# Kernel tuning notes

Measured on AMD Instinct MI355X. Metric: run time of the kernel, lower is better.

The kernel has to match this reference:

```python
import jax, jax.numpy as jnp
import numpy as np
from jax import lax

N = 4096        # num graph nodes
T = 8           # timesteps (LSTM batch dim in original, batch_first=False)
IN_DIM = 64
H = 128         # hidden_dim
OUT_DIM = 1
E_RAND = 65536  # random edges; self-loops appended -> E = 69632


def setup_inputs() -> dict:
    key = jax.random.key(0)
    ks = jax.random.split(key, 18)
    s = 0.05
    f = lambda k, shp: (jax.random.normal(k, shp, jnp.float32) * s)
    src = jnp.concatenate([jax.random.randint(ks[15], (E_RAND,), 0, N), jnp.arange(N)]).astype(jnp.int32)
    dst = jnp.concatenate([jax.random.randint(ks[16], (E_RAND,), 0, N), jnp.arange(N)]).astype(jnp.int32)
    return {
        "input": jax.random.normal(ks[0], (N, T, IN_DIM), jnp.float32),
        "hidden": f(ks[1], (1, T, H)),
        "cell": f(ks[2], (1, T, H)),
        "pre_w": f(ks[3], (IN_DIM, H)),
        "pre_b": f(ks[4], (H,)),
        "w_ih": f(ks[5], (4 * H, H)),
        "w_hh": f(ks[6], (4 * H, H)),
        "b_ih": f(ks[7], (4 * H,)),
        "b_hh": f(ks[8], (4 * H,)),
        "gat_wsrc": f(ks[9], (H, H)),
        "gat_wdst": f(ks[10], (H, H)),
        "gat_attn": f(ks[11], (H,)),
        "gat_b": f(ks[12], (H,)),
        "out_w": f(ks[13], (H, OUT_DIM)),
        "out_b": f(ks[14], (OUT_DIM,)),
        "edge_src": src,
        "edge_dst": dst,
    }


def reference(input, hidden, cell, pre_w, pre_b, w_ih, w_hh, b_ih, b_hh,
              gat_wsrc, gat_wdst, gat_attn, gat_b, out_w, out_b,
              edge_src, edge_dst):
    n_nodes = input.shape[0]
    x = input @ pre_w + pre_b                         # (N, T, H)
    b = b_ih + b_hh

    # LSTM over node dimension (seq = nodes); the T per-timestep runs of the
    # original Python loop are independent (init states come from the given
    # hidden/cell), so we batch them along T.
    def step(carry, x_n):                             # x_n: (T, H)
        h, c = carry
        g = x_n @ w_ih.T + h @ w_hh.T + b             # (T, 4H), torch gate order i,f,g,o
        i_g, f_g, g_g, o_g = jnp.split(g, 4, axis=-1)
        c = jax.nn.sigmoid(f_g) * c + jax.nn.sigmoid(i_g) * jnp.tanh(g_g)
        h = jax.nn.sigmoid(o_g) * jnp.tanh(c)
        return (h, c), h

    (hT, cT), outs = lax.scan(step, (hidden[0], cell[0]), x)   # outs: (N, T, H)

    # GATv2Conv (DGL semantics, num_heads=1, share_weights=False)
    fs = outs @ gat_wsrc                              # (N, T, H)
    fd = outs @ gat_wdst
    e = jax.nn.leaky_relu(fs[edge_src] + fd[edge_dst], 0.2)    # (E, T, H)
    logits = e @ gat_attn                             # (E, T)
    # edge softmax per destination node (numerically stable)
    m = lax.stop_gradient(jax.ops.segment_max(logits, edge_dst, num_segments=n_nodes))
    a = jnp.exp(logits - m[edge_dst])
    denom = jax.ops.segment_sum(a, edge_dst, num_segments=n_nodes)
    alpha = a / denom[edge_dst]                       # (E, T)
    agg = jax.ops.segment_sum(alpha[..., None] * fs[edge_src], edge_dst, num_segments=n_nodes)
    rst = agg + gat_b                                 # (N, T, H)

    # dropout is identity in eval mode
    y = rst @ out_w + out_b                           # (N, T, OUT_DIM)
    return (y, hT[None], cT[None])
```

## Files before the change

### kernel.cpp

```cpp
#include <hip/hip_runtime.h>
#include <hip/hip_bf16.h>

#define N_NODES 4096
#define T_STEPS 8
#define INDIM   64
#define HDIM    128
#define G4      512
#define NROWS   (N_NODES * T_STEPS)
#define LOG2E   1.4426950408889634f

typedef __hip_bfloat16 bf16;
typedef __attribute__((ext_vector_type(8))) short bf16x8;
typedef __attribute__((ext_vector_type(4))) float f32x4;
typedef __attribute__((ext_vector_type(8))) int   i32x8;

__device__ __forceinline__ float asfloat_u(unsigned int u) {
    union { unsigned int i; float f; } v; v.i = u; return v.f;
}
__device__ __forceinline__ float fexp2(float x) {
    float r; asm("v_exp_f32 %0, %1" : "=v"(r) : "v"(x)); return r;
}

#define P_O0 32768
#define P_O1 (P_O0 + 512)
#define P_O2 (P_O1 + 16384)
#define P_O3 (P_O2 + 16384)
#define P_O4 (P_O3 + 128)
#define P_O5 (P_O4 + 1)
#define P_O6 (P_O5 + 65536)
#define P_O7 (P_O6 + 128)
__global__ void prep_kernel(const float* __restrict__ pre_w, const float* __restrict__ pre_b,
                            const float* __restrict__ w_ih, const float* __restrict__ b_ih,
                            const float* __restrict__ b_hh, const float* __restrict__ w_hh,
                            const float* __restrict__ wsrc, const float* __restrict__ wdst,
                            const float* __restrict__ out_w, const float* __restrict__ out_b,
                            const float* __restrict__ gat_b, const float* __restrict__ attn,
                            float* __restrict__ Wc, float* __restrict__ bc,
                            float* __restrict__ wsT, float* __restrict__ wdT,
                            float* __restrict__ wso, float* __restrict__ cy,
                            unsigned char* __restrict__ whh8, float* __restrict__ attn2) {
    int id = blockIdx.x * 256 + threadIdx.x;
    if (id < P_O0) {
        int g = id >> 6, i = id & 63;
        float s = 0.f;
        for (int k = 0; k < HDIM; k++) s += pre_w[i * HDIM + k] * w_ih[g * HDIM + k];
        int gate = g >> 7;
        Wc[id] = s * ((gate == 2) ? -2.f * LOG2E : -LOG2E);
    } else if (id < P_O1) {
        int g = id - P_O0;
        float s = b_ih[g] + b_hh[g];
        for (int k = 0; k < HDIM; k++) s += pre_b[k] * w_ih[g * HDIM + k];
        int gate = g >> 7;
        bc[g] = s * ((gate == 2) ? -2.f * LOG2E : -LOG2E);
    } else if (id < P_O2) {
        int c = id - P_O1;
        int co = c >> 7, k = c & 127;
        wsT[c] = wsrc[k * HDIM + co];
    } else if (id < P_O3) {
        int c = id - P_O2;
        int co = c >> 7, k = c & 127;
        wdT[c] = wdst[k * HDIM + co];
    } else if (id < P_O4) {
        int hi = id - P_O3;
        float s = 0.f;
        for (int ho = 0; ho < HDIM; ho++) s += wsrc[hi * HDIM + ho] * out_w[ho];
        wso[hi] = s;
    } else if (id == P_O4) {
        float s = out_b[0];
        for (int h = 0; h < HDIM; h++) s += gat_b[h] * out_w[h];
        cy[0] = s;
    } else if (id < P_O6) {
        int c = id - P_O5;
        int gate = c >> 14;
        float v = w_hh[c] * ((gate == 2) ? -2.f * LOG2E : -LOG2E);
        int pk = __builtin_amdgcn_cvt_pk_fp8_f32(v, v, 0, false);
        whh8[c] = (unsigned char)(pk & 0xff);
    } else if (id < P_O7) {
        int c = id - P_O6;
        attn2[c] = attn[c] * LOG2E;
    }
}

__global__ __launch_bounds__(512) void xw_kernel(const float* __restrict__ input,
                                                 const float* __restrict__ Wc,
                                                 const float* __restrict__ bc,
                                                 bf16* __restrict__ xw) {
    __shared__ __align__(16) float in_lds[16 * INDIM];
    int tid = threadIdx.x;
    int rowbase = blockIdx.x * 16;
    in_lds[tid]       = input[(size_t)rowbase * INDIM + tid];
    in_lds[tid + 512] = input[(size_t)rowbase * INDIM + tid + 512];
    __syncthreads();
    int g = tid;
    int gate = g >> 7, hh = g & 127;
    float4 w[16];
    const float4* wr = reinterpret_cast<const float4*>(Wc + g * INDIM);
#pragma unroll
    for (int u = 0; u < 16; u++) w[u] = wr[u];
    float b = bc[g];
    for (int r = 0; r < 16; r++) {
        const float4* hv = reinterpret_cast<const float4*>(in_lds + r * INDIM);
        float a0 = b, a1 = 0.f, a2 = 0.f, a3 = 0.f;
#pragma unroll
        for (int u = 0; u < 16; u++) {
            float4 h4 = hv[u]; float4 wv = w[u];
            a0 = fmaf(h4.x, wv.x, a0); a1 = fmaf(h4.y, wv.y, a1);
            a2 = fmaf(h4.z, wv.z, a2); a3 = fmaf(h4.w, wv.w, a3);
        }
        xw[(size_t)(rowbase + r) * G4 + hh * 4 + gate] = __float2bfloat16((a0 + a1) + (a2 + a3));
    }
}

__global__ __launch_bounds__(256, 1) void lstm_kernel(const bf16* __restrict__ xw,
                                                      const unsigned char* __restrict__ whh8,
                                                      const float* __restrict__ hidden0,
                                                      const float* __restrict__ cell0,
                                                      float* __restrict__ outs,
                                                      float* __restrict__ dout,
                                                      const int* __restrict__ esrc,
                                                      const int* __restrict__ edst,
                                                      int nE,
                                                      int* __restrict__ rowptr,
                                                      int* __restrict__ ssrc) {
    __shared__ __align__(16) char hbuf0[2 * 144];
    __shared__ __align__(16) char hbuf1[2 * 144];
    __shared__ int cnt[N_NODES];
    __shared__ int part[256];
    const int tid  = threadIdx.x;

    if (blockIdx.x == 4) {
        for (int i = tid; i < N_NODES; i += 256) cnt[i] = 0;
        __syncthreads();
        for (int i = tid; i < nE; i += 256) atomicAdd(&cnt[edst[i]], 1);
        __syncthreads();
        int base = tid * 16, loc[16], s = 0;
#pragma unroll
        for (int j = 0; j < 16; j++) { loc[j] = s; s += cnt[base + j]; }
        part[tid] = s;
        __syncthreads();
        for (int off = 1; off < 256; off <<= 1) {
            int v = (tid >= off) ? part[tid - off] : 0;
            __syncthreads();
            part[tid] += v;
            __syncthreads();
        }
        int pre = part[tid] - s;
#pragma unroll
        for (int j = 0; j < 16; j++) rowptr[base + j] = pre + loc[j];
        if (tid == 255) rowptr[N_NODES] = nE;
        __syncthreads();
#pragma unroll
        for (int j = 0; j < 16; j++) cnt[base + j] = pre + loc[j];
        __syncthreads();
        for (int i = tid; i < nE; i += 256) {
            int d = edst[i];
            int pos = atomicAdd(&cnt[d], 1);
            ssrc[pos] = esrc[i];
        }
        return;
    }

    const int w    = tid >> 6;
    const int lane = tid & 63;
    const int kg   = lane >> 4;
    const int lr   = lane & 15;
    const int q    = lr & 1;
    const int d    = (lr >> 1) & 3;
    const int b    = lr >> 3;
    const int qg   = blockIdx.x * 2 + q;
    const int hb   = 32 * w + 16 * b + kg * 4 + d;

    i32x8 afr[4][2];
#pragma unroll
    for (int G = 0; G < 4; G++)
#pragma unroll
        for (int bb = 0; bb < 2; bb++) {
            const unsigned char* rowp =
                whh8 + (size_t)(G * 128 + 32 * w + 16 * bb + lr) * HDIM + kg * 32;
            afr[G][bb] = *reinterpret_cast<const i32x8*>(rowp);
        }

    const int roff = q * 144 + kg * 32;
    const int woff = q * 144 + hb;
    const int sc   = 0x7f7f7f7f;

    float cv = cell0[qg * HDIM + hb];
    float hv = hidden0[qg * HDIM + hb];
    {
        int pk = __builtin_amdgcn_cvt_pk_fp8_f32(hv, hv, 0, false);
        *reinterpret_cast<unsigned char*>(hbuf0 + woff) = (unsigned char)(pk & 0xff);
    }

    const uint2* xq = reinterpret_cast<const uint2*>(xw) + qg * 128 + hb;
    float* outp = outs + qg * HDIM + hb;

    uint2 xb[8];
#pragma unroll
    for (int i = 0; i < 8; i++) xb[i] = xq[i * 1024];
    __syncthreads();

#define SEL(M) ((d & 2) ? ((d & 1) ? (M)[3] : (M)[2]) : ((d & 1) ? (M)[1] : (M)[0]))
#define STEPX(NIDX, RB, WB, XQ)                                                      \
    do {                                                                             \
        i32x8 bfr = *reinterpret_cast<const i32x8*>(RB + roff);                      \
        f32x4 z = {0.f, 0.f, 0.f, 0.f};                                              \
        f32x4 a00 = __builtin_amdgcn_mfma_scale_f32_16x16x128_f8f6f4(                \
            afr[0][0], bfr, z, 0, 0, 0, sc, 0, sc);                                  \
        f32x4 a01 = __builtin_amdgcn_mfma_scale_f32_16x16x128_f8f6f4(                \
            afr[0][1], bfr, z, 0, 0, 0, sc, 0, sc);                                  \
        f32x4 a10 = __builtin_amdgcn_mfma_scale_f32_16x16x128_f8f6f4(                \
            afr[1][0], bfr, z, 0, 0, 0, sc, 0, sc);                                  \
        f32x4 a11 = __builtin_amdgcn_mfma_scale_f32_16x16x128_f8f6f4(                \
            afr[1][1], bfr, z, 0, 0, 0, sc, 0, sc);                                  \
        f32x4 a20 = __builtin_amdgcn_mfma_scale_f32_16x16x128_f8f6f4(                \
            afr[2][0], bfr, z, 0, 0, 0, sc, 0, sc);                                  \
        f32x4 a21 = __builtin_amdgcn_mfma_scale_f32_16x16x128_f8f6f4(                \
            afr[2][1], bfr, z, 0, 0, 0, sc, 0, sc);                                  \
        f32x4 a30 = __builtin_amdgcn_mfma_scale_f32_16x16x128_f8f6f4(                \
            afr[3][0], bfr, z, 0, 0, 0, sc, 0, sc);                                  \
        f32x4 a31 = __builtin_amdgcn_mfma_scale_f32_16x16x128_f8f6f4(                \
            afr[3][1], bfr, z, 0, 0, 0, sc, 0, sc);                                  \
        f32x4 m0 = b ? a01 : a00;                                                    \
        f32x4 m1 = b ? a11 : a10;                                                    \
        f32x4 m2 = b ? a21 : a20;                                                    \
        f32x4 m3 = b ? a31 : a30;                                                    \
        float gi = SEL(m0) + asfloat_u((XQ).x << 16);                                \
        float gf = SEL(m1) + asfloat_u((XQ).x & 0xffff0000u);                        \
        float gg = SEL(m2) + asfloat_u((XQ).y << 16);                                \
        float go = SEL(m3) + asfloat_u((XQ).y & 0xffff0000u);                        \
        float A = fexp2(gi), C = fexp2(gf), B = fexp2(gg);                           \
        float p = 1.f + A, r = 1.f + B, s = 1.f + C;                                 \
        float pr = p * r;                                                            \
        float num = fmaf(cv, pr, (2.f - r) * s);                                     \
        cv = num * __builtin_amdgcn_rcpf(pr * s);                                    \
        float O = fexp2(go), F = fexp2(cv * (-2.f * LOG2E));                         \
        float po = 1.f + O, rf = 1.f + F;                                            \
        hv = (2.f - rf) * __builtin_amdgcn_rcpf(po * rf);                            \
        int pk = __builtin_amdgcn_cvt_pk_fp8_f32(hv, hv, 0, false);                  \
        *reinterpret_cast<unsigned char*>(WB + woff) = (unsigned char)(pk & 0xff);   \
        outp[(NIDX) * 1024] = hv;                                                    \
        asm volatile("s_waitcnt lgkmcnt(0)" ::: "memory");                           \
        __builtin_amdgcn_s_barrier();                                                \
        __builtin_amdgcn_sched_barrier(0);                                           \
    } while (0)

    for (int n = 0; n < N_NODES; n += 8) {
#pragma unroll
        for (int i = 0; i < 8; i++) {
            if (i & 1) STEPX(n + i, hbuf1, hbuf0, xb[i]);
            else       STEPX(n + i, hbuf0, hbuf1, xb[i]);
            xb[i] = xq[(n + i + 8) * 1024];
        }
    }
#undef STEPX
#undef SEL

    dout[NROWS + qg * HDIM + hb] = hv;
    dout[NROWS + T_STEPS * HDIM + qg * HDIM + hb] = cv;
}

__global__ __launch_bounds__(256) void fsfd_kernel(const float* __restrict__ outs,
                                                   const float* __restrict__ wsT,
                                                   const float* __restrict__ wdT,
                                                   const float* __restrict__ wso,
                                                   bf16* __restrict__ fs,
                                                   bf16* __restrict__ fd,
                                                   float* __restrict__ fso) {
    __shared__ __align__(16) float rows[32 * HDIM];
    int tid = threadIdx.x;
    size_t base = (size_t)blockIdx.x * 32 * HDIM;
#pragma unroll
    for (int j = 0; j < 16; j++) rows[tid + j * 256] = outs[base + tid + j * 256];
    __syncthreads();
    int c = tid;
    const float4* wT = reinterpret_cast<const float4*>(
        (c < HDIM) ? (wsT + c * HDIM) : (wdT + (c - HDIM) * HDIM));
    float4 w[32];
#pragma unroll
    for (int u = 0; u < 32; u++) w[u] = wT[u];
    bf16* dst = (c < HDIM) ? (fs + base + c) : (fd + base + (c - HDIM));
    for (int r = 0; r < 32; r++) {
        const float4* hv = reinterpret_cast<const float4*>(rows + r * HDIM);
        float a0 = 0.f, a1 = 0.f, a2 = 0.f, a3 = 0.f;
#pragma unroll
        for (int u = 0; u < 32; u++) {
            float4 h4 = hv[u]; float4 wv = w[u];
            a0 = fmaf(h4.x, wv.x, a0); a1 = fmaf(h4.y, wv.y, a1);
            a2 = fmaf(h4.z, wv.z, a2); a3 = fmaf(h4.w, wv.w, a3);
        }
        dst[(size_t)r * HDIM] = __float2bfloat16((a0 + a1) + (a2 + a3));
    }
    if (tid < 32) {
        const float* rp = rows + tid * HDIM;
        float s = 0.f;
        for (int k = 0; k < HDIM; k++) {
            int kk = (k + tid) & 127;
            s += rp[kk] * wso[kk];
        }
        fso[blockIdx.x * 32 + tid] = s;
    }
}

__global__ __launch_bounds__(256) void edge_csr_kernel(const int* __restrict__ ssrc,
                                                       const int* __restrict__ rowptr,
                                                       const bf16* __restrict__ fs,
                                                       const bf16* __restrict__ fd,
                                                       const float* __restrict__ attn2,
                                                       const float* __restrict__ fso,
                                                       const float* __restrict__ cy,
                                                       float* __restrict__ dout) {
    int dn = blockIdx.x * 4 + (threadIdx.x >> 6);
    int l  = threadIdx.x & 63;
    float a0 = attn2[2 * l], a1 = attn2[2 * l + 1];
    const unsigned int* fdp = reinterpret_cast<const unsigned int*>(fd) + (size_t)dn * 512 + l;
    unsigned int fdw[8];
#pragma unroll
    for (int t = 0; t < 8; t++) fdw[t] = fdp[t * 64];
    float den[8], num[8];
#pragma unroll
    for (int t = 0; t < 8; t++) { den[t] = 0.f; num[t] = 0.f; }
    int e0 = rowptr[dn], e1 = rowptr[dn + 1];
    for (int e = e0; e < e1; e++) {
        int s = ssrc[e];
        const unsigned int* fsp = reinterpret_cast<const unsigned int*>(fs) + (size_t)s * 512 + l;
        float4 fsoA = *reinterpret_cast<const float4*>(fso + s * 8);
        float4 fsoB = *reinterpret_cast<const float4*>(fso + s * 8 + 4);
        float fsov[8] = {fsoA.x, fsoA.y, fsoA.z, fsoA.w, fsoB.x, fsoB.y, fsoB.z, fsoB.w};
#pragma unroll
        for (int t = 0; t < 8; t++) {
            unsigned int uf = fsp[t * 64];
            float x1 = asfloat_u(uf << 16) + asfloat_u(fdw[t] << 16);
            float x2 = asfloat_u(uf & 0xffff0000u) + asfloat_u(fdw[t] & 0xffff0000u);
            x1 = fmaxf(x1, 0.f) + 0.2f * fminf(x1, 0.f);
            x2 = fmaxf(x2, 0.f) + 0.2f * fminf(x2, 0.f);
            float v = x1 * a0 + x2 * a1;
#pragma unroll
            for (int m = 32; m >= 1; m >>= 1) v += __shfl_xor(v, m, 64);
            float a = fexp2(v);
            den[t] += a;
            num[t] = fmaf(a, fsov[t], num[t]);
        }
    }
    if (l == 0) {
        float cyv = cy[0];
        float4 y0, y1;
        y0.x = num[0] * __builtin_amdgcn_rcpf(den[0]) + cyv;
        y0.y = num[1] * __builtin_amdgcn_rcpf(den[1]) + cyv;
        y0.z = num[2] * __builtin_amdgcn_rcpf(den[2]) + cyv;
        y0.w = num[3] * __builtin_amdgcn_rcpf(den[3]) + cyv;
        y1.x = num[4] * __builtin_amdgcn_rcpf(den[4]) + cyv;
        y1.y = num[5] * __builtin_amdgcn_rcpf(den[5]) + cyv;
        y1.z = num[6] * __builtin_amdgcn_rcpf(den[6]) + cyv;
        y1.w = num[7] * __builtin_amdgcn_rcpf(den[7]) + cyv;
        *reinterpret_cast<float4*>(dout + dn * 8)     = y0;
        *reinterpret_cast<float4*>(dout + dn * 8 + 4) = y1;
    }
}

extern "C" void kernel_launch(void* const* d_in, const int* in_sizes, int n_in,
                              void* d_out, int out_size, void* d_ws, size_t ws_size,
                              hipStream_t stream) {
    const float* input  = (const float*)d_in[0];
    const float* hidden = (const float*)d_in[1];
    const float* cell   = (const float*)d_in[2];
    const float* pre_w  = (const float*)d_in[3];
    const float* pre_b  = (const float*)d_in[4];
    const float* w_ih   = (const float*)d_in[5];
    const float* w_hh   = (const float*)d_in[6];
    const float* b_ih   = (const float*)d_in[7];
    const float* b_hh   = (const float*)d_in[8];
    const float* wsrc   = (const float*)d_in[9];
    const float* wdst   = (const float*)d_in[10];
    const float* attn   = (const float*)d_in[11];
    const float* gatb   = (const float*)d_in[12];
    const float* outw   = (const float*)d_in[13];
    const float* outb   = (const float*)d_in[14];
    const int*   esrc   = (const int*)d_in[15];
    const int*   edst   = (const int*)d_in[16];
    int nE = in_sizes[15];
    float* dout = (float*)d_out;
    char* ws = (char*)d_ws;

    const size_t o_xw    = 0;
    const size_t o_outs  = 33554432;
    const size_t o_fs    = 50331648;
    const size_t o_fd    = 58720256;
    const size_t o_fso   = 67108864;
    const size_t o_rowptr= 67272704;
    const size_t o_ssrc  = 67289344;
    const size_t o_wc    = 67502080;
    const size_t o_bc    = 67633152;
    const size_t o_wsT   = 67635200;
    const size_t o_wdT   = 67700736;
    const size_t o_wso   = 67766272;
    const size_t o_cy    = 67766784;
    const size_t o_attn2 = 67767040;
    const size_t o_whh8  = o_fs;

    bf16*  xw    = (bf16*)(ws + o_xw);
    float* outs  = (float*)(ws + o_outs);
    bf16*  fs    = (bf16*)(ws + o_fs);
    bf16*  fd    = (bf16*)(ws + o_fd);
    float* fso   = (float*)(ws + o_fso);
    int*   rowptr= (int*)(ws + o_rowptr);
    int*   ssrc  = (int*)(ws + o_ssrc);
    float* Wc    = (float*)(ws + o_wc);
    float* bc    = (float*)(ws + o_bc);
    float* wsT   = (float*)(ws + o_wsT);
    float* wdT   = (float*)(ws + o_wdT);
    float* wso   = (float*)(ws + o_wso);
    float* cy    = (float*)(ws + o_cy);
    float* attn2 = (float*)(ws + o_attn2);
    unsigned char* whh8 = (unsigned char*)(ws + o_whh8);

    prep_kernel<<<516, 256, 0, stream>>>(pre_w, pre_b, w_ih, b_ih, b_hh, w_hh, wsrc, wdst,
                                         outw, outb, gatb, attn,
                                         Wc, bc, wsT, wdT, wso, cy, whh8, attn2);
    xw_kernel<<<2048, 512, 0, stream>>>(input, Wc, bc, xw);
    lstm_kernel<<<5, 256, 0, stream>>>(xw, whh8, hidden, cell, outs, dout,
                                       esrc, edst, nE, rowptr, ssrc);
    fsfd_kernel<<<1024, 256, 0, stream>>>(outs, wsT, wdT, wso, fs, fd, fso);
    edge_csr_kernel<<<N_NODES / 4, 256, 0, stream>>>(ssrc, rowptr, fs, fd, attn2, fso, cy, dout);
}
```

Measured before the change: 1.651 ms.

## Overlap fs/fd projection with LSTM scan via progress-flag consumer blocks

Merges the separate fsfd kernel into the LSTM kernel as 256 extra consumer blocks. Each consumer spins on per-LSTM-block progress counters in global memory and projects 128 nodes of LSTM outputs once they are published. The LSTM blocks publish progress every 256 steps after a fence. This hides the projection work behind the serial recurrence, at the cost of requiring the producer blocks to be co-resident with the spinning consumers, and it adds fence and barrier overhead on the critical LSTM path.

```diff
diff --git a/kernel.cpp b/kernel.cpp
--- a/kernel.cpp
+++ b/kernel.cpp
@@ -29,6 +29,7 @@
 #define P_O5 (P_O4 + 1)
 #define P_O6 (P_O5 + 65536)
 #define P_O7 (P_O6 + 128)
+#define P_O8 (P_O7 + 4)
 __global__ void prep_kernel(const float* __restrict__ pre_w, const float* __restrict__ pre_b,
                             const float* __restrict__ w_ih, const float* __restrict__ b_ih,
                             const float* __restrict__ b_hh, const float* __restrict__ w_hh,
@@ -38,7 +39,8 @@
                             float* __restrict__ Wc, float* __restrict__ bc,
                             float* __restrict__ wsT, float* __restrict__ wdT,
                             float* __restrict__ wso, float* __restrict__ cy,
-                            unsigned char* __restrict__ whh8, float* __restrict__ attn2) {
+                            unsigned char* __restrict__ whh8, float* __restrict__ attn2,
+                            int* __restrict__ progress) {
     int id = blockIdx.x * 256 + threadIdx.x;
     if (id < P_O0) {
         int g = id >> 6, i = id & 63;
@@ -78,6 +80,8 @@
     } else if (id < P_O7) {
         int c = id - P_O6;
         attn2[c] = attn[c] * LOG2E;
+    } else if (id < P_O8) {
+        progress[id - P_O7] = 0;
     }
 }
 
@@ -121,14 +125,21 @@
                                                       const int* __restrict__ edst,
                                                       int nE,
                                                       int* __restrict__ rowptr,
-                                                      int* __restrict__ ssrc) {
-    __shared__ __align__(16) char hbuf0[2 * 144];
-    __shared__ __align__(16) char hbuf1[2 * 144];
-    __shared__ int cnt[N_NODES];
-    __shared__ int part[256];
-    const int tid  = threadIdx.x;
-
-    if (blockIdx.x == 4) {
+                                                      int* __restrict__ ssrc,
+                                                      const float* __restrict__ wsT,
+                                                      const float* __restrict__ wdT,
+                                                      const float* __restrict__ wso,
+                                                      bf16* __restrict__ fs,
+                                                      bf16* __restrict__ fd,
+                                                      float* __restrict__ fso,
+                                                      int* __restrict__ progress) {
+    __shared__ __align__(16) char pool[17408];
+    const int tid = threadIdx.x;
+    const int bid = blockIdx.x;
+
+    if (bid == 4) {
+        int* cnt  = (int*)pool;
+        int* part = (int*)(pool + 16384);
         for (int i = tid; i < N_NODES; i += 256) cnt[i] = 0;
         __syncthreads();
         for (int i = tid; i < nE; i += 256) atomicAdd(&cnt[edst[i]], 1);
@@ -160,6 +171,63 @@
         return;
     }
 
+    if (bid >= 5) {
+        int fb = bid - 5;
+        int target = (fb + 1) * 16;
+        if (tid == 0) {
+            for (;;) {
+                int p0 = __hip_atomic_load(&progress[0], __ATOMIC_RELAXED, __HIP_MEMORY_SCOPE_AGENT);
+                int p1 = __hip_atomic_load(&progress[1], __ATOMIC_RELAXED, __HIP_MEMORY_SCOPE_AGENT);
+                int p2 = __hip_atomic_load(&progress[2], __ATOMIC_RELAXED, __HIP_MEMORY_SCOPE_AGENT);
+                int p3 = __hip_atomic_load(&progress[3], __ATOMIC_RELAXED, __HIP_MEMORY_SCOPE_AGENT);
+                int mn = min(min(p0, p1), min(p2, p3));
+                if (mn >= target) break;
+                __builtin_amdgcn_s_sleep(32);
+            }
+        }
+        __syncthreads();
+        __threadfence();
+        float* rows = (float*)pool;
+        int c = tid;
+        const float4* wT = reinterpret_cast<const float4*>(
+            (c < HDIM) ? (wsT + c * HDIM) : (wdT + (c - HDIM) * HDIM));
+        float4 w[32];
+#pragma unroll
+        for (int u = 0; u < 32; u++) w[u] = wT[u];
+        for (int ch = 0; ch < 4; ch++) {
+            int rowbase = fb * 128 + ch * 32;
+            size_t base = (size_t)rowbase * HDIM;
+            __syncthreads();
+#pragma unroll
+            for (int j = 0; j < 16; j++) rows[tid + j * 256] = outs[base + tid + j * 256];
+            __syncthreads();
+            bf16* dst = (c < HDIM) ? (fs + base + c) : (fd + base + (c - HDIM));
+            for (int r = 0; r < 32; r++) {
+                const float4* hv = reinterpret_cast<const float4*>(rows + r * HDIM);
+                float a0 = 0.f, a1 = 0.f, a2 = 0.f, a3 = 0.f;
+#pragma unroll
+                for (int u = 0; u < 32; u++) {
+                    float4 h4 = hv[u]; float4 wv = w[u];
+                    a0 = fmaf(h4.x, wv.x, a0); a1 = fmaf(h4.y, wv.y, a1);
+                    a2 = fmaf(h4.z, wv.z, a2); a3 = fmaf(h4.w, wv.w, a3);
+                }
+                dst[(size_t)r * HDIM] = __float2bfloat16((a0 + a1) + (a2 + a3));
+            }
+            if (tid < 32) {
+                const float* rp = rows + tid * HDIM;
+                float s = 0.f;
+                for (int k = 0; k < HDIM; k++) {
+                    int kk = (k + tid) & 127;
+                    s += rp[kk] * wso[kk];
+                }
+                fso[rowbase + tid] = s;
+            }
+        }
+        return;
+    }
+
+    char* hbuf0 = pool;
+    char* hbuf1 = pool + 288;
     const int w    = tid >> 6;
     const int lane = tid & 63;
     const int kg   = lane >> 4;
@@ -167,7 +235,7 @@
     const int q    = lr & 1;
     const int d    = (lr >> 1) & 3;
     const int b    = lr >> 3;
-    const int qg   = blockIdx.x * 2 + q;
+    const int qg   = bid * 2 + q;
     const int hb   = 32 * w + 16 * b + kg * 4 + d;
 
     i32x8 afr[4][2];
@@ -251,54 +319,21 @@
             else       STEPX(n + i, hbuf0, hbuf1, xb[i]);
             xb[i] = xq[(n + i + 8) * 1024];
         }
+        if ((n & 255) == 248) {
+            asm volatile("s_waitcnt vmcnt(0)" ::: "memory");
+            __syncthreads();
+            if (tid == 0) {
+                __threadfence();
+                __hip_atomic_store(&progress[bid], n + 8, __ATOMIC_RELAXED,
+                                   __HIP_MEMORY_SCOPE_AGENT);
+            }
+        }
     }
 #undef STEPX
 #undef SEL
 
     dout[NROWS + qg * HDIM + hb] = hv;
     dout[NROWS + T_STEPS * HDIM + qg * HDIM + hb] = cv;
-}
-
-__global__ __launch_bounds__(256) void fsfd_kernel(const float* __restrict__ outs,
-                                                   const float* __restrict__ wsT,
-                                                   const float* __restrict__ wdT,
-                                                   const float* __restrict__ wso,
-                                                   bf16* __restrict__ fs,
-                                                   bf16* __restrict__ fd,
-                                                   float* __restrict__ fso) {
-    __shared__ __align__(16) float rows[32 * HDIM];
-    int tid = threadIdx.x;
-    size_t base = (size_t)blockIdx.x * 32 * HDIM;
-#pragma unroll
-    for (int j = 0; j < 16; j++) rows[tid + j * 256] = outs[base + tid + j * 256];
-    __syncthreads();
-    int c = tid;
-    const float4* wT = reinterpret_cast<const float4*>(
-        (c < HDIM) ? (wsT + c * HDIM) : (wdT + (c - HDIM) * HDIM));
-    float4 w[32];
-#pragma unroll
-    for (int u = 0; u < 32; u++) w[u] = wT[u];
-    bf16* dst = (c < HDIM) ? (fs + base + c) : (fd + base + (c - HDIM));
-    for (int r = 0; r < 32; r++) {
-        const float4* hv = reinterpret_cast<const float4*>(rows + r * HDIM);
-        float a0 = 0.f, a1 = 0.f, a2 = 0.f, a3 = 0.f;
-#pragma unroll
-        for (int u = 0; u < 32; u++) {
-            float4 h4 = hv[u]; float4 wv = w[u];
-            a0 = fmaf(h4.x, wv.x, a0); a1 = fmaf(h4.y, wv.y, a1);
-            a2 = fmaf(h4.z, wv.z, a2); a3 = fmaf(h4.w, wv.w, a3);
-        }
-        dst[(size_t)r * HDIM] = __float2bfloat16((a0 + a1) + (a2 + a3));
-    }
-    if (tid < 32) {
-        const float* rp = rows + tid * HDIM;
-        float s = 0.f;
-        for (int k = 0; k < HDIM; k++) {
-            int kk = (k + tid) & 127;
-            s += rp[kk] * wso[kk];
-        }
-        fso[blockIdx.x * 32 + tid] = s;
-    }
 }
 
 __global__ __launch_bounds__(256) void edge_csr_kernel(const int* __restrict__ ssrc,
@@ -395,6 +430,7 @@
     const size_t o_wso   = 67766272;
     const size_t o_cy    = 67766784;
     const size_t o_attn2 = 67767040;
+    const size_t o_prog  = 67767552;
     const size_t o_whh8  = o_fs;
 
     bf16*  xw    = (bf16*)(ws + o_xw);
@@ -411,14 +447,15 @@
     float* wso   = (float*)(ws + o_wso);
     float* cy    = (float*)(ws + o_cy);
     float* attn2 = (float*)(ws + o_attn2);
+    int*   prog  = (int*)(ws + o_prog);
     unsigned char* whh8 = (unsigned char*)(ws + o_whh8);
 
     prep_kernel<<<516, 256, 0, stream>>>(pre_w, pre_b, w_ih, b_ih, b_hh, w_hh, wsrc, wdst,
                                          outw, outb, gatb, attn,
-                                         Wc, bc, wsT, wdT, wso, cy, whh8, attn2);
+                                         Wc, bc, wsT, wdT, wso, cy, whh8, attn2, prog);
     xw_kernel<<<2048, 512, 0, stream>>>(input, Wc, bc, xw);
-    lstm_kernel<<<5, 256, 0, stream>>>(xw, whh8, hidden, cell, outs, dout,
-                                       esrc, edst, nE, rowptr, ssrc);
-    fsfd_kernel<<<1024, 256, 0, stream>>>(outs, wsT, wdT, wso, fs, fd, fso);
+    lstm_kernel<<<261, 256, 0, stream>>>(xw, whh8, hidden, cell, outs, dout,
+                                         esrc, edst, nE, rowptr, ssrc,
+                                         wsT, wdT, wso, fs, fd, fso, prog);
     edge_csr_kernel<<<N_NODES / 4, 256, 0, stream>>>(ssrc, rowptr, fs, fd, attn2, fso, cy, dout);
 }
```

Measured after the change: 1.707 ms. 3.4% more time.
